# Performance work log

Measured on AMD Instinct MI355X. Metric: run time of the kernel, lower is better.

## Reference

```python
import jax, jax.numpy as jnp
import numpy as np

B, T, DM, H, D = 4, 2048, 1024, 16, 64
INNER = H * D


def setup_inputs() -> dict:
    key = jax.random.key(0)
    ks = jax.random.split(key, 8)
    s = 0.02
    x = jax.random.normal(ks[0], (B, T, DM), dtype=jnp.float32)
    state = jnp.zeros((B, H, D, D), dtype=jnp.float32)
    Wq = jax.random.normal(ks[1], (DM, INNER), dtype=jnp.float32) * s
    Wk = jax.random.normal(ks[2], (DM, INNER), dtype=jnp.float32) * s
    Wv = jax.random.normal(ks[3], (DM, INNER), dtype=jnp.float32) * s
    Wa = jax.random.normal(ks[4], (DM, H), dtype=jnp.float32) * s
    ba = jnp.zeros((H,), dtype=jnp.float32)
    Wb = jax.random.normal(ks[5], (DM, H), dtype=jnp.float32) * s
    bb = jnp.zeros((H,), dtype=jnp.float32)  # beta_init=0.5 -> logit(0.5)=0
    Wo = jax.random.normal(ks[6], (INNER, DM), dtype=jnp.float32) * s
    return {"x": x, "state": state, "Wq": Wq, "Wk": Wk, "Wv": Wv,
            "Wa": Wa, "ba": ba, "Wb": Wb, "bb": bb, "Wo": Wo}


def reference(x, state, Wq, Wk, Wv, Wa, ba, Wb, bb, Wo):
    Bb, Tt, _ = x.shape
    Q = (x @ Wq).reshape(Bb, Tt, H, D)
    K = (x @ Wk).reshape(Bb, Tt, H, D)
    V = (x @ Wv).reshape(Bb, Tt, H, D)
    alpha = jax.nn.sigmoid(x @ Wa + ba)  # (B,T,H) forget gate
    beta = jax.nn.sigmoid(x @ Wb + bb)   # (B,T,H) write gate
    # F.normalize(p=2, dim=-1) with eps=1e-12 clamp on the norm
    K = K / jnp.maximum(jnp.linalg.norm(K, axis=-1, keepdims=True), 1e-12)

    def step(S, inp):
        qt, kt, vt, at, bt = inp  # (B,H,D),(B,H,D),(B,H,D),(B,H),(B,H)
        S = at[..., None, None] * S + bt[..., None, None] * jnp.einsum('bhi,bhj->bhij', vt, kt)
        yt = jnp.einsum('bhij,bhj->bhi', S, qt)
        return S, yt

    xs = (jnp.swapaxes(Q, 0, 1), jnp.swapaxes(K, 0, 1), jnp.swapaxes(V, 0, 1),
          jnp.swapaxes(alpha, 0, 1), jnp.swapaxes(beta, 0, 1))
    S, ys = jax.lax.scan(step, state, xs)  # ys: (T,B,H,D)
    out = jnp.swapaxes(ys, 0, 1).reshape(Bb, Tt, INNER) @ Wo
    return out, S
```

## Files before the change

### kernel.cpp

```cpp
#include <hip/hip_runtime.h>
#include <hip/hip_bf16.h>
#include <math.h>

#define B_SZ   4
#define T_LEN  2048
#define DM     1024
#define NH     16
#define DH     64
#define INNER  1024
#define NROWS  (B_SZ*T_LEN)
#define NQ     (NROWS*INNER)
#define CH     64
#define NCH    (T_LEN/CH)

typedef __bf16 bf16x8 __attribute__((ext_vector_type(8)));
typedef __bf16 bf16x4 __attribute__((ext_vector_type(4)));
typedef float  f32x4  __attribute__((ext_vector_type(4)));
typedef __attribute__((address_space(3))) void*       lds_vp;
typedef const __attribute__((address_space(1))) void* gbl_vp;

__device__ __forceinline__ int swz(int row, int col) {
    return (row << 6) + ((((col >> 3) + (row >> 2)) & 7) << 3) + (col & 7);
}

__global__ __launch_bounds__(256) void wt_cast_transpose(const float* __restrict__ Wq,
                                                         const float* __restrict__ Wk,
                                                         const float* __restrict__ Wv,
                                                         const float* __restrict__ Wo,
                                                         __bf16* __restrict__ WqT,
                                                         __bf16* __restrict__ WkT,
                                                         __bf16* __restrict__ WvT,
                                                         __bf16* __restrict__ WoT) {
    __shared__ float tile[64][65];
    const float* W;
    __bf16* WT;
    if      (blockIdx.z == 0) { W = Wq; WT = WqT; }
    else if (blockIdx.z == 1) { W = Wk; WT = WkT; }
    else if (blockIdx.z == 2) { W = Wv; WT = WvT; }
    else                      { W = Wo; WT = WoT; }

    const int k0 = blockIdx.y * 64, n0 = blockIdx.x * 64;
    const int tr  = threadIdx.x >> 4;
    const int tc4 = (threadIdx.x & 15) * 4;

#pragma unroll
    for (int r = 0; r < 4; r++) {
        const int k = tr + 16 * r;
        const float4 v = *(const float4*)(W + (size_t)(k0 + k) * DM + n0 + tc4);
        tile[k][tc4 + 0] = v.x;
        tile[k][tc4 + 1] = v.y;
        tile[k][tc4 + 2] = v.z;
        tile[k][tc4 + 3] = v.w;
    }
    __syncthreads();
#pragma unroll
    for (int r = 0; r < 4; r++) {
        const int n = tr + 16 * r;
        bf16x4 o;
#pragma unroll
        for (int j = 0; j < 4; j++) o[j] = (__bf16)tile[tc4 + j][n];
        *(bf16x4*)(WT + (size_t)(n0 + n) * DM + k0 + tc4) = o;
    }
}

#define STAGE_STRIDE 24576
#define B_BASE 16384

template <typename CT>
__device__ __forceinline__ void gemm_pipe_body(const __bf16* __restrict__ A,
                                               const __bf16* __restrict__ BT,
                                               CT* __restrict__ C,
                                               int m0, int n0bt, int n0c) {
    __shared__ __align__(16) char lds[3 * STAGE_STRIDE];

    const int tid  = threadIdx.x;
    const int wid  = tid >> 6;
    const int lane = tid & 63;
    const int wm = wid >> 1;
    const int wn = wid & 1;
    const int frow = lane & 15, quad = lane >> 4;

    int offA[8], offB[4];
#pragma unroll
    for (int i = 0; i < 8; ++i) {
        const int ra = wm * 128 + i * 16 + frow;
        offA[i] = ra * 64 + ((quad ^ ((ra >> 1) & 3)) << 4);
    }
#pragma unroll
    for (int j = 0; j < 4; ++j) {
        const int rb = wn * 64 + j * 16 + frow;
        offB[j] = B_BASE + rb * 64 + ((quad ^ ((rb >> 1) & 3)) << 4);
    }

    const int lr = lane >> 2;
    const int cs = ((lane & 3) ^ ((lane >> 3) & 3)) << 3;
    const __bf16* gA[4];
#pragma unroll
    for (int q = 0; q < 4; ++q)
        gA[q] = A + (size_t)(m0 + wid * 64 + q * 16 + lr) * 1024 + cs;
    const __bf16* gB[2];
#pragma unroll
    for (int q = 0; q < 2; ++q)
        gB[q] = BT + (size_t)(n0bt + wid * 32 + q * 16 + lr) * 1024 + cs;

#define STG(t_, b_) do {                                                           \
        _Pragma("unroll")                                                          \
        for (int q_ = 0; q_ < 4; ++q_)                                             \
            __builtin_amdgcn_global_load_lds((gbl_vp)(gA[q_] + (size_t)(t_) * 32), \
                (lds_vp)(lds + (b_) * STAGE_STRIDE + (wid * 64 + q_ * 16) * 64),   \
                16, 0, 0);                                                         \
        _Pragma("unroll")                                                          \
        for (int q_ = 0; q_ < 2; ++q_)                                             \
            __builtin_amdgcn_global_load_lds((gbl_vp)(gB[q_] + (size_t)(t_) * 32), \
                (lds_vp)(lds + (b_) * STAGE_STRIDE + B_BASE + (wid * 32 + q_ * 16) * 64), \
                16, 0, 0);                                                         \
    } while (0)

#define VM6 asm volatile("s_waitcnt vmcnt(6)" ::: "memory")
#define VM0 asm volatile("s_waitcnt vmcnt(0)" ::: "memory")

    f32x4 acc[8][4];
#pragma unroll
    for (int i = 0; i < 8; i++)
#pragma unroll
        for (int j = 0; j < 4; j++) acc[i][j] = (f32x4)0.f;

    STG(0, 0); STG(1, 1);
    VM6;
    asm volatile("s_barrier" ::: "memory");

#define PH(b_, STG_STMT, VM_STMT)                                                  \
    {                                                                              \
        const char* Sb_ = lds + (b_) * STAGE_STRIDE;                               \
        bf16x8 af_[8], bfr_[4];                                                    \
        _Pragma("unroll")                                                          \
        for (int i_ = 0; i_ < 8; ++i_) af_[i_]  = *(const bf16x8*)(Sb_ + offA[i_]);\
        _Pragma("unroll")                                                          \
        for (int j_ = 0; j_ < 4; ++j_) bfr_[j_] = *(const bf16x8*)(Sb_ + offB[j_]);\
        STG_STMT;                                                                  \
        asm volatile("s_barrier" ::: "memory");                                    \
        asm volatile("s_waitcnt lgkmcnt(0)" ::: "memory");                         \
        __builtin_amdgcn_sched_barrier(0);                                         \
        __builtin_amdgcn_s_setprio(1);                                             \
        _Pragma("unroll")                                                          \
        for (int mi_ = 0; mi_ < 8; ++mi_)                                          \
            _Pragma("unroll")                                                      \
            for (int nj_ = 0; nj_ < 4; ++nj_)                                      \
                acc[mi_][nj_] = __builtin_amdgcn_mfma_f32_16x16x32_bf16(           \
                    af_[mi_], bfr_[nj_], acc[mi_][nj_], 0, 0, 0);                  \
        __builtin_amdgcn_s_setprio(0);                                             \
        VM_STMT;                                                                   \
        asm volatile("s_barrier" ::: "memory");                                    \
    }

    for (int u = 0; u < 10; ++u) {
        const int p = 3 * u;
        PH(0, STG(p + 2, 2), VM6);
        PH(1, STG(p + 3, 0), VM6);
        PH(2, STG(p + 4, 1), VM6);
    }
    PH(0, , VM0);
    PH(1, , );

#undef PH
#undef STG
#undef VM6
#undef VM0

    const int cr = quad * 4, cc = frow;
#pragma unroll
    for (int mi = 0; mi < 8; ++mi) {
#pragma unroll
        for (int nj = 0; nj < 4; ++nj) {
            CT* Cp = C + (size_t)(m0 + wm * 128 + mi * 16 + cr) * 1024
                       + n0c + wn * 64 + nj * 16 + cc;
#pragma unroll
            for (int r = 0; r < 4; r++) Cp[(size_t)r * 1024] = (CT)acc[mi][nj][r];
        }
    }
}

__global__ __launch_bounds__(256, 2) void qkv_gemm_8ph(const __bf16* __restrict__ xb,
                                                       const __bf16* __restrict__ BTall,
                                                       __bf16* __restrict__ QKV) {
    const int id = blockIdx.x;
    const int wg = (id & 7) * 96 + (id >> 3);
    const int mt = wg / 24, nt = wg % 24;
    const int mat = nt >> 3;
    gemm_pipe_body<__bf16>(xb, BTall, QKV + (size_t)mat * NQ,
                           mt * 256, nt * 128, (nt & 7) * 128);
}

__global__ __launch_bounds__(256, 2) void out_gemm_8ph(const __bf16* __restrict__ Yb,
                                                       const __bf16* __restrict__ WoT,
                                                       float* __restrict__ Cout) {
    const int id = blockIdx.x;
    const int wg = (id & 7) * 32 + (id >> 3);
    const int mt = wg >> 3, nt = wg & 7;
    gemm_pipe_body<float>(Yb, WoT, Cout, mt * 256, nt * 128, nt * 128);
}

#define WGS 1032
#define LAS 40
__global__ __launch_bounds__(256) void gates_fused(const float* __restrict__ x,
                                                   const float* __restrict__ Wa,
                                                   const float* __restrict__ ba,
                                                   const float* __restrict__ Wb,
                                                   const float* __restrict__ bb,
                                                   float* __restrict__ AlphaT,
                                                   float* __restrict__ BetaT,
                                                   __bf16* __restrict__ xb) {
    __shared__ __align__(16) __bf16 lWg[32 * WGS];
    __shared__ __align__(16) __bf16 lA[64 * LAS];

    const int tid = threadIdx.x;
    const int wid = tid >> 6, lane = tid & 63;
    const int quad = lane >> 4, frow = lane & 15;
    const int m0 = blockIdx.x * 64;

    {
        const int kbase = tid * 4;
#pragma unroll
        for (int j = 0; j < 4; j++) {
            const int k = kbase + j;
            const float4* war = (const float4*)(Wa + (size_t)k * NH);
            const float4* wbr = (const float4*)(Wb + (size_t)k * NH);
#pragma unroll
            for (int q = 0; q < 4; q++) {
                const float4 a = war[q], bq = wbr[q];
                lWg[(q * 4 + 0) * WGS + k] = (__bf16)a.x;
                lWg[(q * 4 + 1) * WGS + k] = (__bf16)a.y;
                lWg[(q * 4 + 2) * WGS + k] = (__bf16)a.z;
                lWg[(q * 4 + 3) * WGS + k] = (__bf16)a.w;
                lWg[(16 + q * 4 + 0) * WGS + k] = (__bf16)bq.x;
                lWg[(16 + q * 4 + 1) * WGS + k] = (__bf16)bq.y;
                lWg[(16 + q * 4 + 2) * WGS + k] = (__bf16)bq.z;
                lWg[(16 + q * 4 + 3) * WGS + k] = (__bf16)bq.w;
            }
        }
    }
    const float bias_a = ba[frow];
    const float bias_b = bb[frow];

    const int rrow = tid >> 2;
    const int rk   = (tid & 3) * 8;
    const float* xrow = x + (size_t)(m0 + rrow) * DM + rk;
    float4 c0 = *(const float4*)(xrow + 0);
    float4 c1 = *(const float4*)(xrow + 4);

    f32x4 acc[2];
    acc[0] = (f32x4)0.f; acc[1] = (f32x4)0.f;

    for (int k0 = 0; k0 < DM; k0 += 32) {
        __syncthreads();
        bf16x8 xv;
        xv[0] = (__bf16)c0.x; xv[1] = (__bf16)c0.y; xv[2] = (__bf16)c0.z; xv[3] = (__bf16)c0.w;
        xv[4] = (__bf16)c1.x; xv[5] = (__bf16)c1.y; xv[6] = (__bf16)c1.z; xv[7] = (__bf16)c1.w;
        *(bf16x8*)&lA[rrow * LAS + rk] = xv;
        *(bf16x8*)(xb + (size_t)(m0 + rrow) * DM + k0 + rk) = xv;
        if (k0 + 32 < DM) {
            c0 = *(const float4*)(xrow + k0 + 32);
            c1 = *(const float4*)(xrow + k0 + 36);
        }
        __syncthreads();
        const bf16x8 af = *(const bf16x8*)&lA[(wid * 16 + frow) * LAS + quad * 8];
#pragma unroll
        for (int ct = 0; ct < 2; ct++) {
            const bf16x8 bf = *(const bf16x8*)&lWg[(ct * 16 + frow) * WGS + k0 + quad * 8];
            acc[ct] = __builtin_amdgcn_mfma_f32_16x16x32_bf16(af, bf, acc[ct], 0, 0, 0);
        }
    }

#pragma unroll
    for (int ct = 0; ct < 2; ct++) {
        const float bias = (ct == 0) ? bias_a : bias_b;
        float* dst = (ct == 0) ? AlphaT : BetaT;
#pragma unroll
        for (int r = 0; r < 4; r++) {
            const int row = m0 + wid * 16 + quad * 4 + r;
            const float s = acc[ct][r] + bias;
            dst[(size_t)frow * NROWS + row] = 1.f / (1.f + __expf(-s));
        }
    }
}

__global__ __launch_bounds__(256) void chunk_ds(const __bf16* __restrict__ Q,
                                                const __bf16* __restrict__ K,
                                                __bf16* __restrict__ V,
                                                const float* __restrict__ AlphaT,
                                                const float* __restrict__ BetaT,
                                                float* __restrict__ Dec,
                                                float* __restrict__ DS,
                                                float* __restrict__ ExpT) {
    __shared__ __align__(16) __bf16 Qb[64 * 64];
    __shared__ __align__(16) __bf16 Kb[64 * 64];
    __shared__ __align__(16) __bf16 KTs[64 * 64];
    __shared__ __align__(16) __bf16 VTb[64 * 64];
    __shared__ __align__(16) __bf16 Ab[64 * 64];
    __shared__ float sla[64], sb[64], swd[64];

    const int blk = blockIdx.x;
    const int c = blk & 31, h = (blk >> 5) & 15, b = blk >> 9;
    const int t0 = c * CH;
    const int tid = threadIdx.x;
    const int wid = tid >> 6, lane = tid & 63;
    const size_t rowbase = ((size_t)(b * T_LEN + t0) * NH + h) * DH;

    const int srow = tid >> 3;
    const int scol = (tid & 7) * 8;
    bf16x8 q8[2], k8[2], v8[2];
#pragma unroll
    for (int r = 0; r < 2; r++) {
        const size_t g = rowbase + (size_t)(srow + 32 * r) * INNER + scol;
        q8[r] = *(const bf16x8*)(Q + g);
        k8[r] = *(const bf16x8*)(K + g);
        v8[r] = *(const bf16x8*)(V + g);
    }

    if (tid < 64) {
        const int t = tid;
        const size_t gaT = (size_t)h * NROWS + b * T_LEN + t0 + t;
        const float a  = AlphaT[gaT];
        const float bt = BetaT[gaT];
        float xx = logf(a);
#pragma unroll
        for (int off = 1; off < 64; off <<= 1) {
            const float y = __shfl_up(xx, off, 64);
            if (t >= off) xx += y;
        }
        const float la63 = __shfl(xx, 63, 64);
        sla[t] = xx;
        sb[t]  = bt;
        swd[t] = bt * __expf(la63 - xx);
        ExpT[gaT] = __expf(xx);
        if (t == 63) Dec[(size_t)(b * NH + h) * NCH + c] = __expf(la63);
    }
    __syncthreads();

#pragma unroll
    for (int r = 0; r < 2; r++) {
        const int row = srow + 32 * r;
        float kf[8];
        float ss = 0.f;
#pragma unroll
        for (int j = 0; j < 8; j++) { kf[j] = (float)k8[r][j]; ss += kf[j] * kf[j]; }
        ss += __shfl_xor(ss, 1, 64);
        ss += __shfl_xor(ss, 2, 64);
        ss += __shfl_xor(ss, 4, 64);
        const float scale = 1.f / fmaxf(sqrtf(ss), 1e-12f);
        const float w = swd[row];
        bf16x8 kn8;
#pragma unroll
        for (int j = 0; j < 8; j++) {
            const float kn = kf[j] * scale;
            kn8[j] = (__bf16)kn;
            KTs[swz(scol + j, row)] = (__bf16)(w * kn);
            VTb[swz(scol + j, row)] = v8[r][j];
        }
        *(bf16x8*)&Qb[swz(row, scol)] = q8[r];
        *(bf16x8*)&Kb[swz(row, scol)] = kn8;
    }
    __syncthreads();

    const int quad = lane >> 4;
    const int frow = lane & 15;
    const int tw = wid * 16;

    f32x4 accG[4];
#pragma unroll
    for (int i = 0; i < 4; i++) accG[i] = (f32x4)0.f;
#pragma unroll
    for (int ks = 0; ks < 2; ks++) {
        const int ko = quad * 8 + 32 * ks;
        const bf16x8 aq = *(const bf16x8*)&Qb[swz(tw + frow, ko)];
#pragma unroll
        for (int st = 0; st < 4; st++) {
            const bf16x8 bk = *(const bf16x8*)&Kb[swz(st * 16 + frow, ko)];
            accG[st] = __builtin_amdgcn_mfma_f32_16x16x32_bf16(aq, bk, accG[st], 0, 0, 0);
        }
    }
#pragma unroll
    for (int st = 0; st < 4; st++) {
#pragma unroll
        for (int r = 0; r < 4; r++) {
            const int t = tw + quad * 4 + r;
            const int s = st * 16 + frow;
            const float av = (s <= t) ? __expf(sla[t] - sla[s]) * sb[s] * accG[st][r] : 0.f;
            Ab[swz(t, s)] = (__bf16)av;
        }
    }
    __syncthreads();

    f32x4 accY[4], accD[4];
#pragma unroll
    for (int i = 0; i < 4; i++) { accY[i] = (f32x4)0.f; accD[i] = (f32x4)0.f; }
#pragma unroll
    for (int ks = 0; ks < 2; ks++) {
        const int ko = quad * 8 + 32 * ks;
        const bf16x8 aA = *(const bf16x8*)&Ab[swz(tw + frow, ko)];
        const bf16x8 aK = *(const bf16x8*)&KTs[swz(tw + frow, ko)];
#pragma unroll
        for (int jt = 0; jt < 4; jt++) {
            const bf16x8 bv = *(const bf16x8*)&VTb[swz(jt * 16 + frow, ko)];
            accY[jt] = __builtin_amdgcn_mfma_f32_16x16x32_bf16(aA, bv, accY[jt], 0, 0, 0);
            accD[jt] = __builtin_amdgcn_mfma_f32_16x16x32_bf16(aK, bv, accD[jt], 0, 0, 0);
        }
    }
#pragma unroll
    for (int jt = 0; jt < 4; jt++) {
#pragma unroll
        for (int r = 0; r < 4; r++) {
            const int row = tw + quad * 4 + r;
            const size_t g = rowbase + (size_t)row * INNER + jt * 16 + frow;
            V[g]  = (__bf16)accY[jt][r];
            DS[g] = accD[jt][r];
        }
    }
}

__global__ __launch_bounds__(256) void state_y(const __bf16* __restrict__ Q,
                                               const float* __restrict__ DS,
                                               const float* __restrict__ Dec,
                                               const float* __restrict__ ExpT,
                                               const float* __restrict__ state_in,
                                               float* __restrict__ state_out,
                                               __bf16* __restrict__ Yb) {
    const int blk = blockIdx.x;
    const int b = blk >> 6, h = (blk >> 2) & 15, iq = blk & 3;
    const int tid = threadIdx.x;
    const int wid = tid >> 6, lane = tid & 63;
    const int frow = lane & 15, quad = lane >> 4;
    const int tw = wid * 16;
    const int i = iq * 16 + frow;

    float S[2][8];
    {
        const float* st = state_in + ((size_t)((b * NH + h) * DH) + i) * DH;
#pragma unroll
        for (int ks = 0; ks < 2; ks++) {
            const int j0 = 32 * ks + quad * 8;
            const float4 a = *(const float4*)(st + j0);
            const float4 d = *(const float4*)(st + j0 + 4);
            S[ks][0] = a.x; S[ks][1] = a.y; S[ks][2] = a.z; S[ks][3] = a.w;
            S[ks][4] = d.x; S[ks][5] = d.y; S[ks][6] = d.z; S[ks][7] = d.w;
        }
    }

    const size_t bh = (size_t)(b * NH + h);
#pragma unroll 2
    for (int c = 0; c < NCH; c++) {
        const int t0 = c * CH;
        const size_t rowbase = ((size_t)(b * T_LEN + t0) * NH + h) * DH;
        const float decay = Dec[bh * NCH + c];

        const bf16x8 aq0 = *(const bf16x8*)(Q + rowbase + (size_t)(tw + frow) * INNER + quad * 8);
        const bf16x8 aq1 = *(const bf16x8*)(Q + rowbase + (size_t)(tw + frow) * INNER + 32 + quad * 8);

        float ds[2][8];
#pragma unroll
        for (int ks = 0; ks < 2; ks++) {
            const int j0 = 32 * ks + quad * 8;
#pragma unroll
            for (int e = 0; e < 8; e++)
                ds[ks][e] = DS[rowbase + (size_t)(j0 + e) * INNER + i];
        }

        bf16x8 bs0, bs1;
#pragma unroll
        for (int e = 0; e < 8; e++) { bs0[e] = (__bf16)S[0][e]; bs1[e] = (__bf16)S[1][e]; }

        f32x4 acc = (f32x4)0.f;
        acc = __builtin_amdgcn_mfma_f32_16x16x32_bf16(aq0, bs0, acc, 0, 0, 0);
        acc = __builtin_amdgcn_mfma_f32_16x16x32_bf16(aq1, bs1, acc, 0, 0, 0);

#pragma unroll
        for (int ks = 0; ks < 2; ks++)
#pragma unroll
            for (int e = 0; e < 8; e++)
                S[ks][e] = decay * S[ks][e] + ds[ks][e];

#pragma unroll
        for (int r = 0; r < 4; r++) {
            const int t = tw + quad * 4 + r;
            const float ee = ExpT[(size_t)h * NROWS + b * T_LEN + t0 + t];
            __bf16* yp = Yb + rowbase + (size_t)t * INNER + i;
            *yp = (__bf16)(ee * acc[r] + (float)*yp);
        }
    }

    float* so = state_out + ((size_t)((b * NH + h) * DH) + i) * DH;
#pragma unroll
    for (int ks = 0; ks < 2; ks++) {
        const int j0 = 32 * ks + quad * 8;
        const float4 v0 = {S[ks][0], S[ks][1], S[ks][2], S[ks][3]};
        const float4 v1 = {S[ks][4], S[ks][5], S[ks][6], S[ks][7]};
        *(float4*)(so + j0)     = v0;
        *(float4*)(so + j0 + 4) = v1;
    }
}

extern "C" void kernel_launch(void* const* d_in, const int* in_sizes, int n_in,
                              void* d_out, int out_size, void* d_ws, size_t ws_size,
                              hipStream_t stream) {
    const float* x     = (const float*)d_in[0];
    const float* state = (const float*)d_in[1];
    const float* Wq    = (const float*)d_in[2];
    const float* Wk    = (const float*)d_in[3];
    const float* Wv    = (const float*)d_in[4];
    const float* Wa    = (const float*)d_in[5];
    const float* ba    = (const float*)d_in[6];
    const float* Wb    = (const float*)d_in[7];
    const float* bb    = (const float*)d_in[8];
    const float* Wo    = (const float*)d_in[9];

    __bf16* Qb    = (__bf16*)d_ws;
    __bf16* Kbf   = Qb + (size_t)NQ;
    __bf16* Vbf   = Kbf + (size_t)NQ;
    float*  DS    = (float*)(Vbf + (size_t)NQ);
    float*  AlphaT= DS + (size_t)NQ;
    float*  BetaT = AlphaT + (size_t)NROWS * NH;
    float*  ExpT  = BetaT + (size_t)NROWS * NH;
    float*  Dec   = ExpT + (size_t)NROWS * NH;
    __bf16* xb    = (__bf16*)(Dec + (size_t)B_SZ * NH * NCH);
    __bf16* WqT   = xb + (size_t)NQ;
    __bf16* WkT   = WqT + (size_t)DM * INNER;
    __bf16* WvT   = WkT + (size_t)DM * INNER;
    __bf16* WoT   = WvT + (size_t)DM * INNER;

    float* out  = (float*)d_out;
    float* Sout = out + (size_t)NQ;

    wt_cast_transpose<<<dim3(16, 16, 4), 256, 0, stream>>>(Wq, Wk, Wv, Wo,
                                                           WqT, WkT, WvT, WoT);
    gates_fused<<<NROWS / 64, 256, 0, stream>>>(x, Wa, ba, Wb, bb,
                                                AlphaT, BetaT, xb);
    qkv_gemm_8ph<<<768, 256, 0, stream>>>(xb, WqT, Qb);
    chunk_ds<<<B_SZ * NH * NCH, 256, 0, stream>>>(Qb, Kbf, Vbf, AlphaT, BetaT,
                                                  Dec, DS, ExpT);
    state_y<<<B_SZ * NH * 4, 256, 0, stream>>>(Qb, DS, Dec, ExpT, state,
                                               Sout, Vbf);
    out_gemm_8ph<<<256, 256, 0, stream>>>(Vbf, WoT, out);
}
```

Before: 262.8 us.

## Restructure bf16 GEMMs to 512-thread 128x256 tiles with 4-stage LDS pipeline

Both bf16 GEMMs (QKV projection and output projection) change from 256-thread blocks with 256x128 tiles and a 3-stage 24KB ring to 512-thread blocks with 128x256 tiles. The new ring is 4 half-k stages in 96KB of LDS, waiting on vmcnt every other phase. Each wave now holds a 64x64 sub-tile with 16 accumulators instead of 32, which lowers register pressure but also lowers MFMA work per LDS read. The larger LDS footprint and launch bounds of (512,1) limit occupancy to one block per CU.

```diff
diff --git a/kernel.cpp b/kernel.cpp
--- a/kernel.cpp
+++ b/kernel.cpp
@@ -63,116 +63,110 @@
     }
 }
 
-#define STAGE_STRIDE 24576
-#define B_BASE 16384
+#define GV2_A(b_, k_) (((b_) * 2 + (k_)) * 8192)
+#define GV2_B(b_, k_) (32768 + ((b_) * 2 + (k_)) * 16384)
 
 template <typename CT>
-__device__ __forceinline__ void gemm_pipe_body(const __bf16* __restrict__ A,
-                                               const __bf16* __restrict__ BT,
-                                               CT* __restrict__ C,
-                                               int m0, int n0bt, int n0c) {
-    __shared__ __align__(16) char lds[3 * STAGE_STRIDE];
+__device__ __forceinline__ void gemm_v2_body(const __bf16* __restrict__ A,
+                                             const __bf16* __restrict__ BT,
+                                             CT* __restrict__ C,
+                                             int m0, int n0bt, int n0c) {
+    __shared__ __align__(16) char lds[98304];
 
     const int tid  = threadIdx.x;
     const int wid  = tid >> 6;
     const int lane = tid & 63;
-    const int wm = wid >> 1;
-    const int wn = wid & 1;
+    const int wm = wid >> 2;
+    const int wn = wid & 3;
     const int frow = lane & 15, quad = lane >> 4;
 
-    int offA[8], offB[4];
-#pragma unroll
-    for (int i = 0; i < 8; ++i) {
-        const int ra = wm * 128 + i * 16 + frow;
-        offA[i] = ra * 64 + ((quad ^ ((ra >> 1) & 3)) << 4);
-    }
+    const int xo = (quad ^ (frow & 3)) << 4;
+    int offA[4], offB[4];
 #pragma unroll
     for (int j = 0; j < 4; ++j) {
-        const int rb = wn * 64 + j * 16 + frow;
-        offB[j] = B_BASE + rb * 64 + ((quad ^ ((rb >> 1) & 3)) << 4);
-    }
-
-    const int lr = lane >> 2;
-    const int cs = ((lane & 3) ^ ((lane >> 3) & 3)) << 3;
-    const __bf16* gA[4];
-#pragma unroll
-    for (int q = 0; q < 4; ++q)
-        gA[q] = A + (size_t)(m0 + wid * 64 + q * 16 + lr) * 1024 + cs;
-    const __bf16* gB[2];
-#pragma unroll
-    for (int q = 0; q < 2; ++q)
-        gB[q] = BT + (size_t)(n0bt + wid * 32 + q * 16 + lr) * 1024 + cs;
-
-#define STG(t_, b_) do {                                                           \
+        offA[j] = (wm * 64 + j * 16 + frow) * 64 + xo;
+        offB[j] = (wn * 64 + j * 16 + frow) * 64 + xo;
+    }
+
+    const int srow = tid >> 2;
+    const int scol = (((tid & 3) ^ (srow & 3)) << 3);
+    const __bf16* srcA  = A  + (size_t)(m0 + srow) * 1024 + scol;
+    const __bf16* srcB0 = BT + (size_t)(n0bt + srow) * 1024 + scol;
+    const __bf16* srcB1 = BT + (size_t)(n0bt + 128 + srow) * 1024 + scol;
+
+#define STGP(as_, bs_, koff_) do {                                                 \
+        __builtin_amdgcn_global_load_lds((gbl_vp)(srcA  + (koff_)),                \
+            (lds_vp)(lds + (as_) + wid * 1024), 16, 0, 0);                         \
+        __builtin_amdgcn_global_load_lds((gbl_vp)(srcB0 + (koff_)),                \
+            (lds_vp)(lds + (bs_) + wid * 1024), 16, 0, 0);                         \
+        __builtin_amdgcn_global_load_lds((gbl_vp)(srcB1 + (koff_)),                \
+            (lds_vp)(lds + (bs_) + 8192 + wid * 1024), 16, 0, 0);                  \
+    } while (0)
+
+#define VM3 asm volatile("s_waitcnt vmcnt(3)" ::: "memory")
+#define VM0 asm volatile("s_waitcnt vmcnt(0)" ::: "memory")
+
+    f32x4 acc[4][4];
+#pragma unroll
+    for (int i = 0; i < 4; i++)
+#pragma unroll
+        for (int j = 0; j < 4; j++) acc[i][j] = (f32x4)0.f;
+
+    STGP(GV2_A(0, 0), GV2_B(0, 0), 0);
+    STGP(GV2_A(0, 1), GV2_B(0, 1), 32);
+    STGP(GV2_A(1, 0), GV2_B(1, 0), 64);
+    VM3;
+    asm volatile("s_barrier" ::: "memory");
+
+#define PH(as_, bs_, STG_STMT, VM_STMT)                                            \
+    {                                                                              \
+        const char* Ab_ = lds + (as_);                                             \
+        const char* Bb_ = lds + (bs_);                                             \
+        bf16x8 af_[4], bf_[4];                                                     \
         _Pragma("unroll")                                                          \
-        for (int q_ = 0; q_ < 4; ++q_)                                             \
-            __builtin_amdgcn_global_load_lds((gbl_vp)(gA[q_] + (size_t)(t_) * 32), \
-                (lds_vp)(lds + (b_) * STAGE_STRIDE + (wid * 64 + q_ * 16) * 64),   \
-                16, 0, 0);                                                         \
-        _Pragma("unroll")                                                          \
-        for (int q_ = 0; q_ < 2; ++q_)                                             \
-            __builtin_amdgcn_global_load_lds((gbl_vp)(gB[q_] + (size_t)(t_) * 32), \
-                (lds_vp)(lds + (b_) * STAGE_STRIDE + B_BASE + (wid * 32 + q_ * 16) * 64), \
-                16, 0, 0);                                                         \
-    } while (0)
-
-#define VM6 asm volatile("s_waitcnt vmcnt(6)" ::: "memory")
-#define VM0 asm volatile("s_waitcnt vmcnt(0)" ::: "memory")
-
-    f32x4 acc[8][4];
-#pragma unroll
-    for (int i = 0; i < 8; i++)
-#pragma unroll
-        for (int j = 0; j < 4; j++) acc[i][j] = (f32x4)0.f;
-
-    STG(0, 0); STG(1, 1);
-    VM6;
-    asm volatile("s_barrier" ::: "memory");
-
-#define PH(b_, STG_STMT, VM_STMT)                                                  \
-    {                                                                              \
-        const char* Sb_ = lds + (b_) * STAGE_STRIDE;                               \
-        bf16x8 af_[8], bfr_[4];                                                    \
-        _Pragma("unroll")                                                          \
-        for (int i_ = 0; i_ < 8; ++i_) af_[i_]  = *(const bf16x8*)(Sb_ + offA[i_]);\
-        _Pragma("unroll")                                                          \
-        for (int j_ = 0; j_ < 4; ++j_) bfr_[j_] = *(const bf16x8*)(Sb_ + offB[j_]);\
+        for (int j_ = 0; j_ < 4; ++j_) {                                           \
+            af_[j_] = *(const bf16x8*)(Ab_ + offA[j_]);                            \
+            bf_[j_] = *(const bf16x8*)(Bb_ + offB[j_]);                            \
+        }                                                                          \
         STG_STMT;                                                                  \
         asm volatile("s_barrier" ::: "memory");                                    \
         asm volatile("s_waitcnt lgkmcnt(0)" ::: "memory");                         \
         __builtin_amdgcn_sched_barrier(0);                                         \
         __builtin_amdgcn_s_setprio(1);                                             \
         _Pragma("unroll")                                                          \
-        for (int mi_ = 0; mi_ < 8; ++mi_)                                          \
+        for (int mi_ = 0; mi_ < 4; ++mi_)                                          \
             _Pragma("unroll")                                                      \
             for (int nj_ = 0; nj_ < 4; ++nj_)                                      \
                 acc[mi_][nj_] = __builtin_amdgcn_mfma_f32_16x16x32_bf16(           \
-                    af_[mi_], bfr_[nj_], acc[mi_][nj_], 0, 0, 0);                  \
+                    af_[mi_], bf_[nj_], acc[mi_][nj_], 0, 0, 0);                   \
         __builtin_amdgcn_s_setprio(0);                                             \
         VM_STMT;                                                                   \
         asm volatile("s_barrier" ::: "memory");                                    \
     }
 
-    for (int u = 0; u < 10; ++u) {
-        const int p = 3 * u;
-        PH(0, STG(p + 2, 2), VM6);
-        PH(1, STG(p + 3, 0), VM6);
-        PH(2, STG(p + 4, 1), VM6);
-    }
-    PH(0, , VM0);
-    PH(1, , );
+    for (int i = 0; i < 7; ++i) {
+        const int kb = i * 128;
+        PH(GV2_A(0, 0), GV2_B(0, 0), STGP(GV2_A(1, 1), GV2_B(1, 1), kb + 96), );
+        PH(GV2_A(0, 1), GV2_B(0, 1), STGP(GV2_A(0, 0), GV2_B(0, 0), kb + 128), VM3);
+        PH(GV2_A(1, 0), GV2_B(1, 0), STGP(GV2_A(0, 1), GV2_B(0, 1), kb + 160), );
+        PH(GV2_A(1, 1), GV2_B(1, 1), STGP(GV2_A(1, 0), GV2_B(1, 0), kb + 192), VM3);
+    }
+    PH(GV2_A(0, 0), GV2_B(0, 0), STGP(GV2_A(1, 1), GV2_B(1, 1), 992), );
+    PH(GV2_A(0, 1), GV2_B(0, 1), , VM0);
+    PH(GV2_A(1, 0), GV2_B(1, 0), , );
+    PH(GV2_A(1, 1), GV2_B(1, 1), , );
 
 #undef PH
-#undef STG
-#undef VM6
+#undef STGP
+#undef VM3
 #undef VM0
 
     const int cr = quad * 4, cc = frow;
 #pragma unroll
-    for (int mi = 0; mi < 8; ++mi) {
+    for (int mi = 0; mi < 4; ++mi) {
 #pragma unroll
         for (int nj = 0; nj < 4; ++nj) {
-            CT* Cp = C + (size_t)(m0 + wm * 128 + mi * 16 + cr) * 1024
+            CT* Cp = C + (size_t)(m0 + wm * 64 + mi * 16 + cr) * 1024
                        + n0c + wn * 64 + nj * 16 + cc;
 #pragma unroll
             for (int r = 0; r < 4; r++) Cp[(size_t)r * 1024] = (CT)acc[mi][nj][r];
@@ -180,24 +174,24 @@
     }
 }
 
-__global__ __launch_bounds__(256, 2) void qkv_gemm_8ph(const __bf16* __restrict__ xb,
-                                                       const __bf16* __restrict__ BTall,
-                                                       __bf16* __restrict__ QKV) {
+__global__ __launch_bounds__(512, 1) void qkv_gemm_v2(const __bf16* __restrict__ xb,
+                                                      const __bf16* __restrict__ BTall,
+                                                      __bf16* __restrict__ QKV) {
     const int id = blockIdx.x;
     const int wg = (id & 7) * 96 + (id >> 3);
-    const int mt = wg / 24, nt = wg % 24;
-    const int mat = nt >> 3;
-    gemm_pipe_body<__bf16>(xb, BTall, QKV + (size_t)mat * NQ,
-                           mt * 256, nt * 128, (nt & 7) * 128);
-}
-
-__global__ __launch_bounds__(256, 2) void out_gemm_8ph(const __bf16* __restrict__ Yb,
-                                                       const __bf16* __restrict__ WoT,
-                                                       float* __restrict__ Cout) {
+    const int mt = wg / 12, nt = wg % 12;
+    const int mat = nt >> 2;
+    gemm_v2_body<__bf16>(xb, BTall, QKV + (size_t)mat * NQ,
+                         mt * 128, nt * 256, (nt & 3) * 256);
+}
+
+__global__ __launch_bounds__(512, 1) void out_gemm_v2(const __bf16* __restrict__ Yb,
+                                                      const __bf16* __restrict__ WoT,
+                                                      float* __restrict__ Cout) {
     const int id = blockIdx.x;
     const int wg = (id & 7) * 32 + (id >> 3);
-    const int mt = wg >> 3, nt = wg & 7;
-    gemm_pipe_body<float>(Yb, WoT, Cout, mt * 256, nt * 128, nt * 128);
+    const int mt = wg >> 2, nt = wg & 3;
+    gemm_v2_body<float>(Yb, WoT, Cout, mt * 128, nt * 256, nt * 256);
 }
 
 #define WGS 1032
@@ -534,10 +528,10 @@
                                                            WqT, WkT, WvT, WoT);
     gates_fused<<<NROWS / 64, 256, 0, stream>>>(x, Wa, ba, Wb, bb,
                                                 AlphaT, BetaT, xb);
-    qkv_gemm_8ph<<<768, 256, 0, stream>>>(xb, WqT, Qb);
+    qkv_gemm_v2<<<768, 512, 0, stream>>>(xb, WqT, Qb);
     chunk_ds<<<B_SZ * NH * NCH, 256, 0, stream>>>(Qb, Kbf, Vbf, AlphaT, BetaT,
                                                   Dec, DS, ExpT);
     state_y<<<B_SZ * NH * 4, 256, 0, stream>>>(Qb, DS, Dec, ExpT, state,
                                                Sout, Vbf);
-    out_gemm_8ph<<<256, 256, 0, stream>>>(Vbf, WoT, out);
-}
+    out_gemm_v2<<<256, 512, 0, stream>>>(Vbf, WoT, out);
+}
```

After: 271.4 us. +3.3%, slower.
